# Performance work log

Hardware: AMD Instinct MI355X
Metric: run time of the kernel (lower is better)

The kernel has to match this reference:

```python
import jax, jax.numpy as jnp
import numpy as np


def setup_inputs() -> dict:
    key = jax.random.key(0)
    k1, k2, k3 = jax.random.split(key, 3)
    K, H = 5, 16
    return {
        "seq_len": 2048,
        "kernel_offsets": jax.random.normal(k1, (K, H), dtype=jnp.float32),
        "kernel_widths": jax.random.normal(k2, (K, H), dtype=jnp.float32),
        "kernel_amplitudes": jax.random.normal(k3, (K, H), dtype=jnp.float32),
    }


def reference(seq_len, kernel_offsets, kernel_widths, kernel_amplitudes):
    # relative offsets: -S .. S inclusive, length 2S+1  (matches torch.arange(-S, S+1))
    rel = jnp.arange(-seq_len, seq_len + 1, dtype=jnp.float32)  # [2S+1]
    # RBF scores per (kernel, head, offset), summed over kernels -> [H, 2S+1]
    diff = kernel_offsets[:, :, None] - rel[None, None, :]        # [K, H, 2S+1]
    rbf = kernel_amplitudes[:, :, None] * jnp.exp(-jnp.abs(kernel_widths)[:, :, None] * diff * diff)
    scores = rbf.sum(axis=0)                                      # [H, 2S+1]
    # Toeplitz index: idx[i, j] = (S-1) + i - j, identical to
    # scipy.linalg.toeplitz(range(S-1, 2S-1), range(S)[::-1]) in the original.
    i = jnp.arange(seq_len)
    idx = (seq_len - 1) + i[:, None] - i[None, :]                 # [S, S], values in [0, 2S-2]
    # gather per head -> [H, S, S]
    return scores[:, idx]
```

## Files before the change

kernel.cpp:

```cpp
#include <hip/hip_runtime.h>
#include <math.h>


#define TI 32
#define BLOCK 256

__global__ __launch_bounds__(BLOCK) void toeplitz_rbf_kernel(
    const float* __restrict__ koff, const float* __restrict__ kwid,
    const float* __restrict__ kamp, float* __restrict__ out,
    int S, int H, int K) {
  extern __shared__ float lds[];
  const int h  = blockIdx.y;
  const int i0 = blockIdx.x * TI;
  const int nscore = S + TI - 1;

  float o0=0,o1=0,o2=0,o3=0,o4=0, w0=0,w1=0,w2=0,w3=0,w4=0, a0=0,a1=0,a2=0,a3=0,a4=0;
  if (K > 0) { o0=koff[0*H+h]; w0=fabsf(kwid[0*H+h]); a0=kamp[0*H+h]; }
  if (K > 1) { o1=koff[1*H+h]; w1=fabsf(kwid[1*H+h]); a1=kamp[1*H+h]; }
  if (K > 2) { o2=koff[2*H+h]; w2=fabsf(kwid[2*H+h]); a2=kamp[2*H+h]; }
  if (K > 3) { o3=koff[3*H+h]; w3=fabsf(kwid[3*H+h]); a3=kamp[3*H+h]; }
  if (K > 4) { o4=koff[4*H+h]; w4=fabsf(kwid[4*H+h]); a4=kamp[4*H+h]; }

  for (int t = threadIdx.x; t < nscore; t += BLOCK) {
    float rel = (float)(i0 + t - S);
    float d0 = o0 - rel, d1 = o1 - rel, d2 = o2 - rel, d3 = o3 - rel, d4 = o4 - rel;
    float s = a0 * __expf(-w0 * d0 * d0)
            + a1 * __expf(-w1 * d1 * d1)
            + a2 * __expf(-w2 * d2 * d2)
            + a3 * __expf(-w3 * d3 * d3)
            + a4 * __expf(-w4 * d4 * d4);
    lds[t] = s;
  }
  __syncthreads();

  const int rows = (S - i0 < TI) ? (S - i0) : TI;

  if (rows == TI && (S & 3) == 0) {
    for (int j = threadIdx.x * 4; j < S; j += BLOCK * 4) {
      const int t0 = S - 1 - j;
      float w[TI + 4];
      #pragma unroll
      for (int m = 0; m < (TI + 4) / 4; ++m)
        *(float4*)&w[4 * m] = *(const float4*)&lds[(t0 - 3) + 4 * m];

      float* __restrict__ p = out + ((size_t)h * S + i0) * (size_t)S + j;
      #pragma unroll
      for (int di = 0; di < TI; ++di) {
        *(float4*)p = make_float4(w[di + 3], w[di + 2], w[di + 1], w[di]);
        p += S;
      }
    }
  } else {
    for (int idx = threadIdx.x; idx < rows * S; idx += BLOCK) {
      int di = idx / S;
      int j  = idx - di * S;
      out[((size_t)h * S + (size_t)(i0 + di)) * (size_t)S + j] =
          lds[(S - 1) + di - j];
    }
  }
}

extern "C" void kernel_launch(void* const* d_in, const int* in_sizes, int n_in,
                              void* d_out, int out_size, void* d_ws, size_t ws_size,
                              hipStream_t stream) {
  const float* koff = (const float*)d_in[1];
  const float* kwid = (const float*)d_in[2];
  const float* kamp = (const float*)d_in[3];
  float* out = (float*)d_out;

  const int K = 5;
  int H = (n_in > 1 && in_sizes[1] > 0) ? in_sizes[1] / K : 16;
  if (H <= 0) H = 16;
  long long ss = (long long)out_size / H;
  int S = (int)(sqrt((double)ss) + 0.5);

  dim3 grid((S + TI - 1) / TI, H);
  size_t lds_bytes = (size_t)(S + TI) * sizeof(float);
  toeplitz_rbf_kernel<<<grid, BLOCK, lds_bytes, stream>>>(koff, kwid, kamp, out, S, H, K);
}
```

Measured before the change: 262.3 us.

## Precompute four shifted reversed score tables and stream rows via aligned float4 copies

Adds a two-kernel path. The first kernel builds four reversed score tables per head, one for each alignment phase, into workspace. The second copies each output row as contiguous aligned float4 loads from the matching table. This replaces the per-thread LDS window gather and element reversal with plain streaming copies, at the cost of an extra launch and an L2-resident table read. The old kernel stays as a fallback when S is not a multiple of four or the workspace is too small.

```diff
diff --git a/kernel.cpp b/kernel.cpp
--- a/kernel.cpp
+++ b/kernel.cpp
@@ -2,8 +2,53 @@
 #include <math.h>
 
 
+#define BLOCK 256
 #define TI 32
-#define BLOCK 256
+
+__global__ __launch_bounds__(BLOCK) void build_tables_kernel(
+    const float* __restrict__ koff, const float* __restrict__ kwid,
+    const float* __restrict__ kamp, float* __restrict__ tbl,
+    int S, int H, int K, int tstride) {
+  const int c = blockIdx.x;
+  const int h = blockIdx.y;
+
+  float o0=0,o1=0,o2=0,o3=0,o4=0, w0=0,w1=0,w2=0,w3=0,w4=0, a0=0,a1=0,a2=0,a3=0,a4=0;
+  if (K > 0) { o0=koff[0*H+h]; w0=fabsf(kwid[0*H+h]); a0=kamp[0*H+h]; }
+  if (K > 1) { o1=koff[1*H+h]; w1=fabsf(kwid[1*H+h]); a1=kamp[1*H+h]; }
+  if (K > 2) { o2=koff[2*H+h]; w2=fabsf(kwid[2*H+h]); a2=kamp[2*H+h]; }
+  if (K > 3) { o3=koff[3*H+h]; w3=fabsf(kwid[3*H+h]); a3=kamp[3*H+h]; }
+  if (K > 4) { o4=koff[4*H+h]; w4=fabsf(kwid[4*H+h]); a4=kamp[4*H+h]; }
+
+  float* __restrict__ dst = tbl + ((size_t)h * 4 + c) * (size_t)tstride;
+  const int n = 2 * S - 1;
+  for (int t = threadIdx.x; t < n; t += BLOCK) {
+    int idx = 2 * S - 2 - t - c;
+    if (idx < 0) continue;
+    float rel = (float)(idx - S);
+    float d0 = o0 - rel, d1 = o1 - rel, d2 = o2 - rel, d3 = o3 - rel, d4 = o4 - rel;
+    dst[t] = a0 * __expf(-w0 * d0 * d0)
+           + a1 * __expf(-w1 * d1 * d1)
+           + a2 * __expf(-w2 * d2 * d2)
+           + a3 * __expf(-w3 * d3 * d3)
+           + a4 * __expf(-w4 * d4 * d4);
+  }
+}
+
+__global__ __launch_bounds__(BLOCK) void row_copy_kernel(
+    const float* __restrict__ tbl, float* __restrict__ out,
+    int S, int tstride) {
+  const int h = blockIdx.y;
+  for (int i = blockIdx.x; i < S; i += gridDim.x) {
+    const int base = S - 1 - i;
+    const int c = base & 3;
+    const float* __restrict__ src =
+        tbl + ((size_t)h * 4 + c) * (size_t)tstride + (base - c);
+    float* __restrict__ dst = out + ((size_t)h * S + i) * (size_t)S;
+    for (int j = threadIdx.x * 4; j < S; j += BLOCK * 4) {
+      *(float4*)(dst + j) = *(const float4*)(src + j);
+    }
+  }
+}
 
 __global__ __launch_bounds__(BLOCK) void toeplitz_rbf_kernel(
     const float* __restrict__ koff, const float* __restrict__ kwid,
@@ -24,17 +69,15 @@
   for (int t = threadIdx.x; t < nscore; t += BLOCK) {
     float rel = (float)(i0 + t - S);
     float d0 = o0 - rel, d1 = o1 - rel, d2 = o2 - rel, d3 = o3 - rel, d4 = o4 - rel;
-    float s = a0 * __expf(-w0 * d0 * d0)
-            + a1 * __expf(-w1 * d1 * d1)
-            + a2 * __expf(-w2 * d2 * d2)
-            + a3 * __expf(-w3 * d3 * d3)
-            + a4 * __expf(-w4 * d4 * d4);
-    lds[t] = s;
+    lds[t] = a0 * __expf(-w0 * d0 * d0)
+           + a1 * __expf(-w1 * d1 * d1)
+           + a2 * __expf(-w2 * d2 * d2)
+           + a3 * __expf(-w3 * d3 * d3)
+           + a4 * __expf(-w4 * d4 * d4);
   }
   __syncthreads();
 
   const int rows = (S - i0 < TI) ? (S - i0) : TI;
-
   if (rows == TI && (S & 3) == 0) {
     for (int j = threadIdx.x * 4; j < S; j += BLOCK * 4) {
       const int t0 = S - 1 - j;
@@ -42,7 +85,6 @@
       #pragma unroll
       for (int m = 0; m < (TI + 4) / 4; ++m)
         *(float4*)&w[4 * m] = *(const float4*)&lds[(t0 - 3) + 4 * m];
-
       float* __restrict__ p = out + ((size_t)h * S + i0) * (size_t)S + j;
       #pragma unroll
       for (int di = 0; di < TI; ++di) {
@@ -74,7 +116,19 @@
   long long ss = (long long)out_size / H;
   int S = (int)(sqrt((double)ss) + 0.5);
 
-  dim3 grid((S + TI - 1) / TI, H);
-  size_t lds_bytes = (size_t)(S + TI) * sizeof(float);
-  toeplitz_rbf_kernel<<<grid, BLOCK, lds_bytes, stream>>>(koff, kwid, kamp, out, S, H, K);
+  const int tstride = (2 * S + 8) & ~3;
+  const size_t ws_needed = (size_t)H * 4 * (size_t)tstride * sizeof(float);
+
+  if ((S & 3) == 0 && d_ws != nullptr && ws_size >= ws_needed) {
+    dim3 g1(4, H);
+    build_tables_kernel<<<g1, BLOCK, 0, stream>>>(koff, kwid, kamp,
+                                                  (float*)d_ws, S, H, K, tstride);
+    int gx = (S >= 512) ? 512 : S;
+    dim3 g2(gx, H);
+    row_copy_kernel<<<g2, BLOCK, 0, stream>>>((const float*)d_ws, out, S, tstride);
+  } else {
+    dim3 grid((S + TI - 1) / TI, H);
+    size_t lds_bytes = (size_t)(S + TI) * sizeof(float);
+    toeplitz_rbf_kernel<<<grid, BLOCK, lds_bytes, stream>>>(koff, kwid, kamp, out, S, H, K);
+  }
 }
```

New measurement: 266.9 us. Within noise of the previous version (+1.7%).
